# Optimization experiments

Hardware: AMD Instinct MI355X
Metric: run time of the kernel (lower is better)

## Reference

```python
import jax, jax.numpy as jnp
import numpy as np

H = 32          # query heads
KV = 8          # kv heads
DH = 64         # head dim
WINDOW = 1024   # sliding window
BASE = 10000.0  # rope base


def _rope(x, pos):
    """Interleaved RoPE as in RotaryEmbedding.apply. x: (B,H,T,Dh), pos: (T,)."""
    inv = 1.0 / (BASE ** (jnp.arange(0, DH, 2, dtype=jnp.float32) / DH))  # (Dh/2,)
    freqs = pos.astype(jnp.float32)[:, None] * inv[None, :]               # (T, Dh/2)
    cos = jnp.cos(freqs)[None, None].astype(x.dtype)
    sin = jnp.sin(freqs)[None, None].astype(x.dtype)
    x1, x2 = x[..., ::2], x[..., 1::2]
    o1 = x1 * cos - x2 * sin
    o2 = x1 * sin + x2 * cos
    return jnp.stack([o1, o2], axis=-1).reshape(x.shape)


def setup_inputs() -> dict:
    key = jax.random.key(0)
    ks = jax.random.split(key, 5)
    B, T, D, Tc = 2, 4096, 2048, 4096
    x = jax.random.normal(ks[0], (B, T, D), jnp.float32)
    k_cache = jax.random.normal(ks[1], (B, KV, Tc, DH), jnp.float32)
    v_cache = jax.random.normal(ks[2], (B, KV, Tc, DH), jnp.float32)
    Wq = jax.random.normal(ks[3], (D, D), jnp.float32) * 0.02
    Wo = jax.random.normal(ks[4], (D, D), jnp.float32) * 0.02
    return {"x": x, "k_cache": k_cache, "v_cache": v_cache, "Wq": Wq, "Wo": Wo}


def reference(x, k_cache, v_cache, Wq, Wo):
    """AttnLayer.forward, role='follower', local=True, return_attn=False, eval mode."""
    B, T, D = x.shape
    rep = H // KV
    # q projection: nn.Linear(d, H*Dh, bias=False) -> x @ W.T
    q = (x @ Wq.T).reshape(B, T, H, DH).transpose(0, 2, 1, 3)  # (B,H,T,Dh)
    Tc = k_cache.shape[2]
    pos_q = jnp.arange(Tc - T, Tc)
    q = _rope(q, pos_q)
    # GQA: KV -> H head replication (repeat_interleave along head dim)
    k = jnp.repeat(k_cache, rep, axis=1)  # (B,H,Tc,Dh)
    v = jnp.repeat(v_cache, rep, axis=1)
    # sliding-window slice: keep last `window` keys
    w = min(WINDOW, Tc)
    k = k[:, :, Tc - w:, :]  # (B,H,Tk,Dh)
    v = v[:, :, Tc - w:, :]
    Tk = w
    scale = 1.0 / np.sqrt(DH).astype(np.float32)
    scores = jnp.einsum('bhtd,bhsd->bhts', q, k) * scale  # (B,H,T,Tk)
    # torch SDPA is_causal with L != S uses a TOP-LEFT aligned tril mask: j <= i
    causal = jnp.arange(Tk)[None, :] <= jnp.arange(T)[:, None]  # (T,Tk)
    scores = jnp.where(causal[None, None], scores, -jnp.inf)
    attn = jax.nn.softmax(scores, axis=-1)
    out = jnp.einsum('bhts,bhsd->bhtd', attn, v)
    out = out.transpose(0, 2, 1, 3).reshape(B, T, H * DH)
    return out @ Wo.T
```

## Files before the change

kernel.cpp:

```cpp
#include <hip/hip_runtime.h>
#include <math.h>

typedef __attribute__((ext_vector_type(8))) short short8;
typedef __attribute__((ext_vector_type(4))) float floatx4;
typedef __attribute__((ext_vector_type(4))) unsigned int uintx4;
typedef __attribute__((ext_vector_type(2))) unsigned int uintx2;

#define MFMA16(a, b, c) __builtin_amdgcn_mfma_f32_16x16x32_bf16((a), (b), (c), 0, 0, 0)

#define QSCALE 0.18033688011112042f

__device__ __forceinline__ unsigned short f2bf(float x) {
    unsigned int u = __float_as_uint(x);
    u += 0x7fffu + ((u >> 16) & 1u);
    return (unsigned short)(u >> 16);
}

__device__ __forceinline__ short8 lds8(const unsigned short* p) {
    return *reinterpret_cast<const short8*>(p);
}

__device__ __forceinline__ void g2l16(const unsigned short* g, unsigned short* l) {
    __builtin_amdgcn_global_load_lds(
        (const __attribute__((address_space(1))) unsigned int*)g,
        (__attribute__((address_space(3))) unsigned int*)l,
        16, 0, 0);
}

__device__ __forceinline__ unsigned int cvtpk(float a, float b) {
    unsigned int r;
    asm("v_cvt_pk_bf16_f32 %0, %1, %2" : "=v"(r) : "v"(a), "v"(b));
    return r;
}

__device__ __forceinline__ void pl32swap(unsigned int& a, unsigned int& b) {
    asm("v_permlane32_swap_b32 %0, %1" : "+v"(a), "+v"(b));
}

__device__ __forceinline__ void pl16swap(unsigned int& a, unsigned int& b) {
    asm("v_permlane16_swap_b32 %0, %1" : "+v"(a), "+v"(b));
}

__global__ void cvt_bf16(const float* __restrict__ src, unsigned short* __restrict__ dst, int n4) {
    int i = blockIdx.x * blockDim.x + threadIdx.x;
    if (i >= n4) return;
    float4 v = reinterpret_cast<const float4*>(src)[i];
    ushort4 o;
    o.x = f2bf(v.x); o.y = f2bf(v.y); o.z = f2bf(v.z); o.w = f2bf(v.w);
    reinterpret_cast<ushort4*>(dst)[i] = o;
}

__global__ void prep_k(const float* __restrict__ kc, unsigned short* __restrict__ Kw) {
    int i = blockIdx.x * blockDim.x + threadIdx.x;
    int d4  = (i & 15) * 4;
    int s   = (i >> 4) & 1023;
    int bkv = i >> 14;
    size_t src = ((size_t)bkv * 4096 + 3072 + s) * 64 + d4;
    float4 kv = *reinterpret_cast<const float4*>(kc + src);
    ushort4 ko;
    ko.x = f2bf(kv.x); ko.y = f2bf(kv.y); ko.z = f2bf(kv.z); ko.w = f2bf(kv.w);
    *reinterpret_cast<ushort4*>(Kw + ((size_t)bkv * 1024 + s) * 64 + d4) = ko;
}

__global__ void prep_v(const float* __restrict__ vc, unsigned short* __restrict__ Vt) {
    __shared__ unsigned short tl[64][72];
    const int bkv = blockIdx.x >> 4;
    const int s0  = (blockIdx.x & 15) * 64;
    const int t   = threadIdx.x;
    const int sl  = t >> 2;
    const int dq  = (t & 3) * 16;
    const float* src = vc + ((size_t)bkv * 4096 + 3072 + s0 + sl) * 64 + dq;
    float4 v0 = reinterpret_cast<const float4*>(src)[0];
    float4 v1 = reinterpret_cast<const float4*>(src)[1];
    float4 v2 = reinterpret_cast<const float4*>(src)[2];
    float4 v3 = reinterpret_cast<const float4*>(src)[3];
    tl[dq +  0][sl] = f2bf(v0.x); tl[dq +  1][sl] = f2bf(v0.y);
    tl[dq +  2][sl] = f2bf(v0.z); tl[dq +  3][sl] = f2bf(v0.w);
    tl[dq +  4][sl] = f2bf(v1.x); tl[dq +  5][sl] = f2bf(v1.y);
    tl[dq +  6][sl] = f2bf(v1.z); tl[dq +  7][sl] = f2bf(v1.w);
    tl[dq +  8][sl] = f2bf(v2.x); tl[dq +  9][sl] = f2bf(v2.y);
    tl[dq + 10][sl] = f2bf(v2.z); tl[dq + 11][sl] = f2bf(v2.w);
    tl[dq + 12][sl] = f2bf(v3.x); tl[dq + 13][sl] = f2bf(v3.y);
    tl[dq + 14][sl] = f2bf(v3.z); tl[dq + 15][sl] = f2bf(v3.w);
    __syncthreads();
    const int dl = t >> 2;
    const int sc = (t & 3) * 16;
    unsigned short* dst = Vt + ((size_t)bkv * 64 + dl) * 1024 + s0 + sc;
    short8 x0 = *reinterpret_cast<const short8*>(&tl[dl][sc]);
    short8 x1 = *reinterpret_cast<const short8*>(&tl[dl][sc + 8]);
    *reinterpret_cast<short8*>(dst)     = x0;
    *reinterpret_cast<short8*>(dst + 8) = x1;
}

template <int EPI>
__global__ __launch_bounds__(512, 2)
void gemm256(const unsigned short* __restrict__ A,
             const unsigned short* __restrict__ Bt,
             float* __restrict__ Cf,
             unsigned short* __restrict__ Cb) {
    constexpr int K  = 2048;
    constexpr int NT = 64;
    __shared__ unsigned short sm[32768];

    const int tid  = threadIdx.x;
    const int lane = tid & 63;
    const int l15  = lane & 15;
    const int quad = lane >> 4;
    const int wid  = tid >> 6;
    const int wr   = wid >> 2;
    const int wc   = wid & 3;

    const int bn = blockIdx.x & 7;
    const int bm = blockIdx.x >> 3;

    const unsigned short* gA0 = A  + (size_t)(bm * 256 + 2 * wid * 16 + l15) * K + quad * 8;
    const unsigned short* gA1 = gA0 + (size_t)16 * K;
    const unsigned short* gB0 = Bt + (size_t)(bn * 256 + 2 * wid * 16 + l15) * K + quad * 8;
    const unsigned short* gB1 = gB0 + (size_t)16 * K;

    auto STAGE = [&](int t) {
        unsigned short* dst = sm + (t & 1) * 16384 + 2 * wid * 512;
        const int off = t * 32;
        g2l16(gA0 + off, dst);
        g2l16(gA1 + off, dst + 512);
        g2l16(gB0 + off, dst + 8192);
        g2l16(gB1 + off, dst + 8704);
    };

    floatx4 acc[8][4];
#pragma unroll
    for (int i = 0; i < 8; ++i)
#pragma unroll
        for (int j = 0; j < 4; ++j) acc[i][j] = floatx4{0, 0, 0, 0};

    STAGE(0);
    STAGE(1);
    asm volatile("s_waitcnt vmcnt(4)" ::: "memory");
    __builtin_amdgcn_s_barrier();
    asm volatile("" ::: "memory");

    for (int t = 0; t < NT; ++t) {
        const unsigned short* cb = sm + (t & 1) * 16384;

        short8 bf[4], af[8];
#pragma unroll
        for (int j = 0; j < 4; ++j)
            bf[j] = lds8(cb + 8192 + (wc * 4 + j) * 512 + lane * 8);
#pragma unroll
        for (int i = 0; i < 8; ++i)
            af[i] = lds8(cb + (wr * 8 + i) * 512 + lane * 8);

        asm volatile("s_waitcnt lgkmcnt(0)" ::: "memory");
        __builtin_amdgcn_s_barrier();
        asm volatile("" ::: "memory");

        if (t + 2 < NT) STAGE(t + 2);

        __builtin_amdgcn_s_setprio(1);
#pragma unroll
        for (int i = 0; i < 8; ++i)
#pragma unroll
            for (int j = 0; j < 4; ++j)
                acc[i][j] = MFMA16(af[i], bf[j], acc[i][j]);
        __builtin_amdgcn_s_setprio(0);

        if (t + 2 < NT) asm volatile("s_waitcnt vmcnt(4)" ::: "memory");
        else            asm volatile("s_waitcnt vmcnt(0)" ::: "memory");
        __builtin_amdgcn_s_barrier();
        asm volatile("" ::: "memory");
    }

    float2* tabf = reinterpret_cast<float2*>(sm);
    if (EPI == 0) {
        const int t0 = (bm & 15) * 256;
        for (int e = tid; e < 8192; e += 512) {
            int tl = e >> 5, d2 = e & 31;
            float f = (float)(t0 + tl) * exp2f(-(float)d2 * 0.41524101186092f);
            float sn, cs; __sincosf(f, &sn, &cs);
            tabf[tl * 32 + d2] = make_float2(cs, sn);
        }
        __syncthreads();
    }

#pragma unroll
    for (int i = 0; i < 8; ++i)
#pragma unroll
        for (int j = 0; j < 4; ++j)
#pragma unroll
            for (int r = 0; r < 4; ++r) {
                int row = bm * 256 + wr * 128 + i * 16 + quad * 4 + r;
                int col = bn * 256 + wc * 64 + j * 16 + l15;
                float v = acc[i][j][r];
                if (EPI == 0) {
                    float p = __shfl_xor(v, 1);
                    int t_ = row & 4095, b_ = row >> 12;
                    int hh = col >> 6, d = col & 63;
                    int tl = wr * 128 + i * 16 + quad * 4 + r;
                    float2 cspair = tabf[tl * 32 + (d >> 1)];
                    float o = (d & 1) ? (p * cspair.y + v * cspair.x)
                                      : (v * cspair.x - p * cspair.y);
                    o *= QSCALE;
                    float po = __shfl_xor(o, 1);
                    if (!(lane & 1)) {
                        unsigned int pk = (unsigned int)f2bf(o) |
                                          ((unsigned int)f2bf(po) << 16);
                        *reinterpret_cast<unsigned int*>(
                            Cb + ((size_t)((b_ * 32 + hh) * 4096 + t_)) * 64 + d) = pk;
                    }
                } else {
                    Cf[(size_t)row * 2048 + col] = v;
                }
            }
}

__global__ __launch_bounds__(512, 8)
void attn(const unsigned short* __restrict__ Q,
          const unsigned short* __restrict__ Kw,
          const unsigned short* __restrict__ Vt,
          unsigned short* __restrict__ O) {
    const int blk  = blockIdx.x;
    const int qblk = blk & 31;
    const int bh   = blk >> 5;
    const int h    = bh & 31;
    const int b    = bh >> 5;
    const int kvh  = h >> 2;

    const int tid  = threadIdx.x;
    const int lane = tid & 63;
    const int l15  = lane & 15;
    const int quad = lane >> 4;
    const int wid  = tid >> 6;
    const int qt0  = qblk * 128 + wid * 16;

    const unsigned short* Qp = Q  + ((size_t)bh * 4096 + qt0) * 64;
    const unsigned short* Kp = Kw + (size_t)(b * 8 + kvh) * 1024 * 64;
    const unsigned short* Vp = Vt + (size_t)(b * 8 + kvh) * 64 * 1024;

    __shared__ unsigned short Ks[2][4096];
    __shared__ unsigned short Vs[2][4096];

    short8 qa0 = lds8(&Qp[l15 * 64 + quad * 8]);
    short8 qa1 = lds8(&Qp[l15 * 64 + 32 + quad * 8]);

    short8 ones;
#pragma unroll
    for (int i = 0; i < 8; ++i) ones[i] = (short)0x3F80;

    const unsigned short* gK = Kp + (size_t)((wid >> 1) * 16 + l15) * 64
                                  + (wid & 1) * 32 + quad * 8;
    const unsigned short* gV = Vp + (size_t)((wid >> 1) * 16 + l15) * 1024
                                  + (wid & 1) * 32 + quad * 8;
    unsigned short* sK0 = &Ks[0][wid * 512];
    unsigned short* sK1 = &Ks[1][wid * 512];
    unsigned short* sV0 = &Vs[0][wid * 512];
    unsigned short* sV1 = &Vs[1][wid * 512];

    const int ntiles = (qblk < 7 ? 2 * qblk + 2 : 16);
    const int nkW    = (qt0 + 16 < 1024) ? qt0 + 16 : 1024;
    const int ntW    = (nkW + 63) >> 6;
    const bool diagW = (qt0 < 1024);

    g2l16(gK, sK0);
    g2l16(gV, sV0);

    floatx4 o0 = {0,0,0,0}, o1 = {0,0,0,0}, o2 = {0,0,0,0}, o3 = {0,0,0,0};
    floatx4 La = {0,0,0,0};
    float m = -INFINITY;

    for (int it = 0; it < ntiles; ++it) {
        __syncthreads();
        const int cur = it & 1;
        if (it + 1 < ntiles) {
            g2l16(gK + (it + 1) * 4096, cur ? sK0 : sK1);
            g2l16(gV + (it + 1) * 64,   cur ? sV0 : sV1);
        }
        if (it >= ntW) continue;
        const int s0 = it << 6;
        const unsigned short* Kc = Ks[cur];
        const unsigned short* Vc = Vs[cur];

        floatx4 sS[4];
        __builtin_amdgcn_s_setprio(1);
#pragma unroll
        for (int c = 0; c < 4; ++c) {
            floatx4 z = {0, 0, 0, 0};
            z = MFMA16(lds8(Kc + c * 1024 + lane * 8), qa0, z);
            z = MFMA16(lds8(Kc + c * 1024 + 512 + lane * 8), qa1, z);
            sS[c] = z;
        }
        __builtin_amdgcn_s_setprio(0);

        const bool last = (it == ntW - 1);
        bool skipHi = false;
        if (last && diagW) {
#pragma unroll
            for (int c = 0; c < 4; ++c)
#pragma unroll
                for (int r = 0; r < 4; ++r)
                    if (s0 + c * 16 + quad * 4 + r > qt0 + l15) sS[c][r] = -INFINITY;
            skipHi = (nkW - s0 <= 32);
        }

        float t0 = fmaxf(fmaxf(sS[0][0], sS[0][1]), fmaxf(sS[0][2], sS[0][3]));
        float t1 = fmaxf(fmaxf(sS[1][0], sS[1][1]), fmaxf(sS[1][2], sS[1][3]));
        float t2 = fmaxf(fmaxf(sS[2][0], sS[2][1]), fmaxf(sS[2][2], sS[2][3]));
        float t3 = fmaxf(fmaxf(sS[3][0], sS[3][1]), fmaxf(sS[3][2], sS[3][3]));
        float mx = fmaxf(fmaxf(t0, t1), fmaxf(t2, t3));
        mx = fmaxf(mx, __shfl_xor(mx, 16));
        mx = fmaxf(mx, __shfl_xor(mx, 32));

        if (!__all(mx <= m + 8.0f)) {
            const float mn = fmaxf(m, mx);
            const float alpha = exp2f(m - mn);
            m = mn;
            o0 *= alpha; o1 *= alpha; o2 *= alpha; o3 *= alpha;
            La *= alpha;
        }

        float p[4][4];
#pragma unroll
        for (int c = 0; c < 4; ++c)
#pragma unroll
            for (int r = 0; r < 4; ++r) p[c][r] = exp2f(sS[c][r] - m);

        unsigned int a0 = cvtpk(p[0][0], p[0][1]);
        unsigned int a1 = cvtpk(p[0][2], p[0][3]);
        unsigned int a2 = cvtpk(p[1][0], p[1][1]);
        unsigned int a3 = cvtpk(p[1][2], p[1][3]);
        pl32swap(a0, a2); pl32swap(a1, a3);
        pl16swap(a0, a2); pl16swap(a1, a3);
        uintx4 tlo = {a0, a1, a2, a3};
        short8 pa_lo = __builtin_bit_cast(short8, tlo);

        __builtin_amdgcn_s_setprio(1);
        o0 = MFMA16(lds8(Vc + 0 * 512 + lane * 8), pa_lo, o0);
        o1 = MFMA16(lds8(Vc + 2 * 512 + lane * 8), pa_lo, o1);
        o2 = MFMA16(lds8(Vc + 4 * 512 + lane * 8), pa_lo, o2);
        o3 = MFMA16(lds8(Vc + 6 * 512 + lane * 8), pa_lo, o3);
        La = MFMA16(ones, pa_lo, La);
        __builtin_amdgcn_s_setprio(0);
        if (!skipHi) {
            unsigned int b0 = cvtpk(p[2][0], p[2][1]);
            unsigned int b1 = cvtpk(p[2][2], p[2][3]);
            unsigned int b2 = cvtpk(p[3][0], p[3][1]);
            unsigned int b3 = cvtpk(p[3][2], p[3][3]);
            pl32swap(b0, b2); pl32swap(b1, b3);
            pl16swap(b0, b2); pl16swap(b1, b3);
            uintx4 thi = {b0, b1, b2, b3};
            short8 pa_hi = __builtin_bit_cast(short8, thi);
            __builtin_amdgcn_s_setprio(1);
            o0 = MFMA16(lds8(Vc + 1 * 512 + lane * 8), pa_hi, o0);
            o1 = MFMA16(lds8(Vc + 3 * 512 + lane * 8), pa_hi, o1);
            o2 = MFMA16(lds8(Vc + 5 * 512 + lane * 8), pa_hi, o2);
            o3 = MFMA16(lds8(Vc + 7 * 512 + lane * 8), pa_hi, o3);
            La = MFMA16(ones, pa_hi, La);
            __builtin_amdgcn_s_setprio(0);
        }
    }

    const float inv = 1.f / La[0];

    unsigned short* Op = O + (size_t)b * 4096 * 2048 + (size_t)(qt0 + l15) * 2048
                           + h * 64 + quad * 4;
    uintx2 w0, w1, w2, w3;
    w0.x = cvtpk(o0[0] * inv, o0[1] * inv); w0.y = cvtpk(o0[2] * inv, o0[3] * inv);
    w1.x = cvtpk(o1[0] * inv, o1[1] * inv); w1.y = cvtpk(o1[2] * inv, o1[3] * inv);
    w2.x = cvtpk(o2[0] * inv, o2[1] * inv); w2.y = cvtpk(o2[2] * inv, o2[3] * inv);
    w3.x = cvtpk(o3[0] * inv, o3[1] * inv); w3.y = cvtpk(o3[2] * inv, o3[3] * inv);
    *reinterpret_cast<uintx2*>(Op)      = w0;
    *reinterpret_cast<uintx2*>(Op + 16) = w1;
    *reinterpret_cast<uintx2*>(Op + 32) = w2;
    *reinterpret_cast<uintx2*>(Op + 48) = w3;
}

extern "C" void kernel_launch(void* const* d_in, const int* in_sizes, int n_in,
                              void* d_out, int out_size, void* d_ws, size_t ws_size,
                              hipStream_t stream) {
    const float* x  = (const float*)d_in[0];
    const float* kc = (const float*)d_in[1];
    const float* vc = (const float*)d_in[2];
    const float* Wq = (const float*)d_in[3];
    const float* Wo = (const float*)d_in[4];
    float* out = (float*)d_out;

    char* ws = (char*)d_ws;
    unsigned short* Xb  = (unsigned short*)(ws);
    unsigned short* Qb  = (unsigned short*)(ws + 33554432);
    unsigned short* Wqb = (unsigned short*)(ws + 67108864);
    unsigned short* Wob = (unsigned short*)(ws + 75497472);
    unsigned short* Kwb = (unsigned short*)(ws + 83886080);
    unsigned short* Vtb = (unsigned short*)(ws + 85983232);

    cvt_bf16<<<16384, 256, 0, stream>>>(x,  Xb,  4194304);
    cvt_bf16<<<4096,  256, 0, stream>>>(Wq, Wqb, 1048576);
    cvt_bf16<<<4096,  256, 0, stream>>>(Wo, Wob, 1048576);
    prep_k<<<1024, 256, 0, stream>>>(kc, Kwb);
    prep_v<<<256, 256, 0, stream>>>(vc, Vtb);

    gemm256<0><<<256, 512, 0, stream>>>(Xb, Wqb, nullptr, Qb);
    attn<<<2048, 512, 0, stream>>>(Qb, Kwb, Vtb, Xb);
    gemm256<1><<<256, 512, 0, stream>>>(Xb, Wob, out, nullptr);
}
```

Measured before the change: 442.2 us.

## Restructure GEMM main loop into finer-grained interleaved load/MFMA stages with 64-wide K tiles

```diff
diff --git a/kernel.cpp b/kernel.cpp
--- a/kernel.cpp
+++ b/kernel.cpp
@@ -94,13 +94,13 @@
 
 template <int EPI>
 __global__ __launch_bounds__(512, 2)
-void gemm256(const unsigned short* __restrict__ A,
-             const unsigned short* __restrict__ Bt,
-             float* __restrict__ Cf,
-             unsigned short* __restrict__ Cb) {
-    constexpr int K  = 2048;
-    constexpr int NT = 64;
-    __shared__ unsigned short sm[32768];
+void gemmk(const unsigned short* __restrict__ A,
+           const unsigned short* __restrict__ Bt,
+           float* __restrict__ Cf,
+           unsigned short* __restrict__ Cb) {
+    constexpr int K   = 2048;
+    constexpr int NKT = 32;
+    __shared__ __align__(16) unsigned short sm[65536];
 
     const int tid  = threadIdx.x;
     const int lane = tid & 63;
@@ -113,19 +113,13 @@
     const int bn = blockIdx.x & 7;
     const int bm = blockIdx.x >> 3;
 
-    const unsigned short* gA0 = A  + (size_t)(bm * 256 + 2 * wid * 16 + l15) * K + quad * 8;
-    const unsigned short* gA1 = gA0 + (size_t)16 * K;
-    const unsigned short* gB0 = Bt + (size_t)(bn * 256 + 2 * wid * 16 + l15) * K + quad * 8;
-    const unsigned short* gB1 = gB0 + (size_t)16 * K;
-
-    auto STAGE = [&](int t) {
-        unsigned short* dst = sm + (t & 1) * 16384 + 2 * wid * 512;
-        const int off = t * 32;
-        g2l16(gA0 + off, dst);
-        g2l16(gA1 + off, dst + 512);
-        g2l16(gB0 + off, dst + 8192);
-        g2l16(gB1 + off, dst + 8704);
-    };
+    const unsigned short* gAl = A  + (size_t)(bm * 256 + l15) * K + quad * 8;
+    const unsigned short* gBl = Bt + (size_t)(bn * 256 + l15) * K + quad * 8;
+
+#define STG_A(kt, kh, c) g2l16(gAl + (size_t)((c) * 8 + wid) * 16 * K + (kt) * 64 + (kh) * 32, \
+                               sm + ((kt) & 1) * 16384 + (kh) * 8192 + ((c) * 8 + wid) * 512)
+#define STG_B(kt, kh, c) g2l16(gBl + (size_t)((c) * 8 + wid) * 16 * K + (kt) * 64 + (kh) * 32, \
+                               sm + 32768 + ((kt) & 1) * 16384 + (kh) * 8192 + ((c) * 8 + wid) * 512)
 
     floatx4 acc[8][4];
 #pragma unroll
@@ -133,42 +127,110 @@
 #pragma unroll
         for (int j = 0; j < 4; ++j) acc[i][j] = floatx4{0, 0, 0, 0};
 
-    STAGE(0);
-    STAGE(1);
-    asm volatile("s_waitcnt vmcnt(4)" ::: "memory");
+    STG_B(0, 0, 0); STG_B(0, 0, 1); STG_A(0, 0, 0); STG_A(0, 0, 1);
+    STG_B(0, 1, 0); STG_B(0, 1, 1); STG_A(0, 1, 0); STG_A(0, 1, 1);
+    STG_B(1, 0, 0); STG_B(1, 0, 1); STG_A(1, 0, 0); STG_A(1, 0, 1);
+    asm volatile("s_waitcnt vmcnt(8)" ::: "memory");
     __builtin_amdgcn_s_barrier();
     asm volatile("" ::: "memory");
 
-    for (int t = 0; t < NT; ++t) {
-        const unsigned short* cb = sm + (t & 1) * 16384;
-
-        short8 bf[4], af[8];
-#pragma unroll
-        for (int j = 0; j < 4; ++j)
-            bf[j] = lds8(cb + 8192 + (wc * 4 + j) * 512 + lane * 8);
-#pragma unroll
-        for (int i = 0; i < 8; ++i)
-            af[i] = lds8(cb + (wr * 8 + i) * 512 + lane * 8);
-
-        asm volatile("s_waitcnt lgkmcnt(0)" ::: "memory");
-        __builtin_amdgcn_s_barrier();
-        asm volatile("" ::: "memory");
-
-        if (t + 2 < NT) STAGE(t + 2);
-
-        __builtin_amdgcn_s_setprio(1);
-#pragma unroll
-        for (int i = 0; i < 8; ++i)
-#pragma unroll
-            for (int j = 0; j < 4; ++j)
-                acc[i][j] = MFMA16(af[i], bf[j], acc[i][j]);
-        __builtin_amdgcn_s_setprio(0);
-
-        if (t + 2 < NT) asm volatile("s_waitcnt vmcnt(4)" ::: "memory");
-        else            asm volatile("s_waitcnt vmcnt(0)" ::: "memory");
-        __builtin_amdgcn_s_barrier();
-        asm volatile("" ::: "memory");
+#define DO_MFMA(ip)                                                  \
+    __builtin_amdgcn_s_setprio(1);                                   \
+    acc[2*(ip)][0]   = MFMA16(af0, bf[0], acc[2*(ip)][0]);           \
+    acc[2*(ip)][1]   = MFMA16(af0, bf[1], acc[2*(ip)][1]);           \
+    acc[2*(ip)][2]   = MFMA16(af0, bf[2], acc[2*(ip)][2]);           \
+    acc[2*(ip)][3]   = MFMA16(af0, bf[3], acc[2*(ip)][3]);           \
+    acc[2*(ip)+1][0] = MFMA16(af1, bf[0], acc[2*(ip)+1][0]);         \
+    acc[2*(ip)+1][1] = MFMA16(af1, bf[1], acc[2*(ip)+1][1]);         \
+    acc[2*(ip)+1][2] = MFMA16(af1, bf[2], acc[2*(ip)+1][2]);         \
+    acc[2*(ip)+1][3] = MFMA16(af1, bf[3], acc[2*(ip)+1][3]);         \
+    __builtin_amdgcn_s_setprio(0);
+
+#define BAR()   { __builtin_amdgcn_s_barrier(); asm volatile("" ::: "memory"); }
+#define LGKM0() asm volatile("s_waitcnt lgkmcnt(0)" ::: "memory")
+
+    for (int kt = 0; kt < NKT; ++kt) {
+        const int d = kt & 1;
+        const unsigned short* Ab = sm + d * 16384;
+        const unsigned short* Bb = sm + 32768 + d * 16384;
+        const bool s1 = (kt + 1 < NKT);
+        const bool s2 = (kt + 2 < NKT);
+        short8 af0, af1, bf[4];
+
+        bf[0] = lds8(Bb + (wc * 4 + 0) * 512 + lane * 8);
+        bf[1] = lds8(Bb + (wc * 4 + 1) * 512 + lane * 8);
+        bf[2] = lds8(Bb + (wc * 4 + 2) * 512 + lane * 8);
+        bf[3] = lds8(Bb + (wc * 4 + 3) * 512 + lane * 8);
+        af0   = lds8(Ab + (wr * 8 + 0) * 512 + lane * 8);
+        af1   = lds8(Ab + (wr * 8 + 1) * 512 + lane * 8);
+        if (s1) STG_B(kt + 1, 1, 0);
+        BAR(); LGKM0();
+        DO_MFMA(0);
+        BAR();
+
+        af0 = lds8(Ab + (wr * 8 + 2) * 512 + lane * 8);
+        af1 = lds8(Ab + (wr * 8 + 3) * 512 + lane * 8);
+        if (s1) STG_B(kt + 1, 1, 1);
+        BAR(); LGKM0();
+        DO_MFMA(1);
+        BAR();
+
+        af0 = lds8(Ab + (wr * 8 + 4) * 512 + lane * 8);
+        af1 = lds8(Ab + (wr * 8 + 5) * 512 + lane * 8);
+        if (s1) STG_A(kt + 1, 1, 0);
+        BAR(); LGKM0();
+        DO_MFMA(2);
+        BAR();
+
+        af0 = lds8(Ab + (wr * 8 + 6) * 512 + lane * 8);
+        af1 = lds8(Ab + (wr * 8 + 7) * 512 + lane * 8);
+        if (s1) STG_A(kt + 1, 1, 1);
+        BAR(); LGKM0();
+        DO_MFMA(3);
+        if (s1) asm volatile("s_waitcnt vmcnt(8)" ::: "memory");
+        else    asm volatile("s_waitcnt vmcnt(0)" ::: "memory");
+        BAR();
+
+        bf[0] = lds8(Bb + 8192 + (wc * 4 + 0) * 512 + lane * 8);
+        bf[1] = lds8(Bb + 8192 + (wc * 4 + 1) * 512 + lane * 8);
+        bf[2] = lds8(Bb + 8192 + (wc * 4 + 2) * 512 + lane * 8);
+        bf[3] = lds8(Bb + 8192 + (wc * 4 + 3) * 512 + lane * 8);
+        af0   = lds8(Ab + 8192 + (wr * 8 + 0) * 512 + lane * 8);
+        af1   = lds8(Ab + 8192 + (wr * 8 + 1) * 512 + lane * 8);
+        if (s2) STG_B(kt + 2, 0, 0);
+        BAR(); LGKM0();
+        DO_MFMA(0);
+        BAR();
+
+        af0 = lds8(Ab + 8192 + (wr * 8 + 2) * 512 + lane * 8);
+        af1 = lds8(Ab + 8192 + (wr * 8 + 3) * 512 + lane * 8);
+        if (s2) STG_B(kt + 2, 0, 1);
+        BAR(); LGKM0();
+        DO_MFMA(1);
+        BAR();
+
+        af0 = lds8(Ab + 8192 + (wr * 8 + 4) * 512 + lane * 8);
+        af1 = lds8(Ab + 8192 + (wr * 8 + 5) * 512 + lane * 8);
+        if (s2) STG_A(kt + 2, 0, 0);
+        BAR(); LGKM0();
+        DO_MFMA(2);
+        BAR();
+
+        af0 = lds8(Ab + 8192 + (wr * 8 + 6) * 512 + lane * 8);
+        af1 = lds8(Ab + 8192 + (wr * 8 + 7) * 512 + lane * 8);
+        if (s2) STG_A(kt + 2, 0, 1);
+        BAR(); LGKM0();
+        DO_MFMA(3);
+        if (s2)      asm volatile("s_waitcnt vmcnt(8)" ::: "memory");
+        else if (s1) asm volatile("s_waitcnt vmcnt(4)" ::: "memory");
+        else         asm volatile("s_waitcnt vmcnt(0)" ::: "memory");
+        BAR();
     }
+#undef STG_A
+#undef STG_B
+#undef DO_MFMA
+#undef BAR
+#undef LGKM0
 
     float2* tabf = reinterpret_cast<float2*>(sm);
     if (EPI == 0) {
@@ -397,7 +459,7 @@
     prep_k<<<1024, 256, 0, stream>>>(kc, Kwb);
     prep_v<<<256, 256, 0, stream>>>(vc, Vtb);
 
-    gemm256<0><<<256, 512, 0, stream>>>(Xb, Wqb, nullptr, Qb);
+    gemmk<0><<<256, 512, 0, stream>>>(Xb, Wqb, nullptr, Qb);
     attn<<<2048, 512, 0, stream>>>(Qb, Kwb, Vtb, Xb);
-    gemm256<1><<<256, 512, 0, stream>>>(Xb, Wob, out, nullptr);
-}
+    gemmk<1><<<256, 512, 0, stream>>>(Xb, Wob, out, nullptr);
+}
```

After: 442.0 us. Within noise of the previous version (-0.0%).

## Shrink GEMM tile to 128x256 for more blocks and split attention launch

Applied to the files above, without the earlier changes.

```diff
diff --git a/kernel.cpp b/kernel.cpp
--- a/kernel.cpp
+++ b/kernel.cpp
@@ -93,14 +93,14 @@
 }
 
 template <int EPI>
-__global__ __launch_bounds__(512, 2)
-void gemm256(const unsigned short* __restrict__ A,
+__global__ __launch_bounds__(512, 4)
+void gemm128(const unsigned short* __restrict__ A,
              const unsigned short* __restrict__ Bt,
              float* __restrict__ Cf,
              unsigned short* __restrict__ Cb) {
     constexpr int K  = 2048;
     constexpr int NT = 64;
-    __shared__ unsigned short sm[32768];
+    __shared__ __align__(16) unsigned short sm[24576];
 
     const int tid  = threadIdx.x;
     const int lane = tid & 63;
@@ -113,42 +113,40 @@
     const int bn = blockIdx.x & 7;
     const int bm = blockIdx.x >> 3;
 
-    const unsigned short* gA0 = A  + (size_t)(bm * 256 + 2 * wid * 16 + l15) * K + quad * 8;
-    const unsigned short* gA1 = gA0 + (size_t)16 * K;
-    const unsigned short* gB0 = Bt + (size_t)(bn * 256 + 2 * wid * 16 + l15) * K + quad * 8;
-    const unsigned short* gB1 = gB0 + (size_t)16 * K;
+    const unsigned short* gA0 = A  + (size_t)(bm * 128 + wid * 16 + l15) * K + quad * 8;
+    const unsigned short* gB0 = Bt + (size_t)(bn * 256 + wid * 16 + l15) * K + quad * 8;
+    const unsigned short* gB1 = gB0 + (size_t)128 * K;
 
     auto STAGE = [&](int t) {
-        unsigned short* dst = sm + (t & 1) * 16384 + 2 * wid * 512;
+        unsigned short* dst = sm + (t & 1) * 12288;
         const int off = t * 32;
-        g2l16(gA0 + off, dst);
-        g2l16(gA1 + off, dst + 512);
-        g2l16(gB0 + off, dst + 8192);
-        g2l16(gB1 + off, dst + 8704);
+        g2l16(gA0 + off, dst + wid * 512);
+        g2l16(gB0 + off, dst + 4096 + wid * 512);
+        g2l16(gB1 + off, dst + 8192 + wid * 512);
     };
 
-    floatx4 acc[8][4];
-#pragma unroll
-    for (int i = 0; i < 8; ++i)
+    floatx4 acc[4][4];
+#pragma unroll
+    for (int i = 0; i < 4; ++i)
 #pragma unroll
         for (int j = 0; j < 4; ++j) acc[i][j] = floatx4{0, 0, 0, 0};
 
     STAGE(0);
     STAGE(1);
-    asm volatile("s_waitcnt vmcnt(4)" ::: "memory");
+    asm volatile("s_waitcnt vmcnt(3)" ::: "memory");
     __builtin_amdgcn_s_barrier();
     asm volatile("" ::: "memory");
 
     for (int t = 0; t < NT; ++t) {
-        const unsigned short* cb = sm + (t & 1) * 16384;
-
-        short8 bf[4], af[8];
+        const unsigned short* cb = sm + (t & 1) * 12288;
+
+        short8 af[4], bf[4];
+#pragma unroll
+        for (int i = 0; i < 4; ++i)
+            af[i] = lds8(cb + (wr * 4 + i) * 512 + lane * 8);
 #pragma unroll
         for (int j = 0; j < 4; ++j)
-            bf[j] = lds8(cb + 8192 + (wc * 4 + j) * 512 + lane * 8);
-#pragma unroll
-        for (int i = 0; i < 8; ++i)
-            af[i] = lds8(cb + (wr * 8 + i) * 512 + lane * 8);
+            bf[j] = lds8(cb + 4096 + (wc * 4 + j) * 512 + lane * 8);
 
         asm volatile("s_waitcnt lgkmcnt(0)" ::: "memory");
         __builtin_amdgcn_s_barrier();
@@ -158,13 +156,13 @@
 
         __builtin_amdgcn_s_setprio(1);
 #pragma unroll
-        for (int i = 0; i < 8; ++i)
+        for (int i = 0; i < 4; ++i)
 #pragma unroll
             for (int j = 0; j < 4; ++j)
                 acc[i][j] = MFMA16(af[i], bf[j], acc[i][j]);
         __builtin_amdgcn_s_setprio(0);
 
-        if (t + 2 < NT) asm volatile("s_waitcnt vmcnt(4)" ::: "memory");
+        if (t + 2 < NT) asm volatile("s_waitcnt vmcnt(3)" ::: "memory");
         else            asm volatile("s_waitcnt vmcnt(0)" ::: "memory");
         __builtin_amdgcn_s_barrier();
         asm volatile("" ::: "memory");
@@ -172,8 +170,8 @@
 
     float2* tabf = reinterpret_cast<float2*>(sm);
     if (EPI == 0) {
-        const int t0 = (bm & 15) * 256;
-        for (int e = tid; e < 8192; e += 512) {
+        const int t0 = (bm & 31) * 128;
+        for (int e = tid; e < 4096; e += 512) {
             int tl = e >> 5, d2 = e & 31;
             float f = (float)(t0 + tl) * exp2f(-(float)d2 * 0.41524101186092f);
             float sn, cs; __sincosf(f, &sn, &cs);
@@ -183,19 +181,19 @@
     }
 
 #pragma unroll
-    for (int i = 0; i < 8; ++i)
+    for (int i = 0; i < 4; ++i)
 #pragma unroll
         for (int j = 0; j < 4; ++j)
 #pragma unroll
             for (int r = 0; r < 4; ++r) {
-                int row = bm * 256 + wr * 128 + i * 16 + quad * 4 + r;
+                int row = bm * 128 + wr * 64 + i * 16 + quad * 4 + r;
                 int col = bn * 256 + wc * 64 + j * 16 + l15;
                 float v = acc[i][j][r];
                 if (EPI == 0) {
                     float p = __shfl_xor(v, 1);
                     int t_ = row & 4095, b_ = row >> 12;
                     int hh = col >> 6, d = col & 63;
-                    int tl = wr * 128 + i * 16 + quad * 4 + r;
+                    int tl = wr * 64 + i * 16 + quad * 4 + r;
                     float2 cspair = tabf[tl * 32 + (d >> 1)];
                     float o = (d & 1) ? (p * cspair.y + v * cspair.x)
                                       : (v * cspair.x - p * cspair.y);
@@ -217,8 +215,8 @@
 void attn(const unsigned short* __restrict__ Q,
           const unsigned short* __restrict__ Kw,
           const unsigned short* __restrict__ Vt,
-          unsigned short* __restrict__ O) {
-    const int blk  = blockIdx.x;
+          unsigned short* __restrict__ O, int base) {
+    const int blk  = blockIdx.x + base;
     const int qblk = blk & 31;
     const int bh   = blk >> 5;
     const int h    = bh & 31;
@@ -397,7 +395,8 @@
     prep_k<<<1024, 256, 0, stream>>>(kc, Kwb);
     prep_v<<<256, 256, 0, stream>>>(vc, Vtb);
 
-    gemm256<0><<<256, 512, 0, stream>>>(Xb, Wqb, nullptr, Qb);
-    attn<<<2048, 512, 0, stream>>>(Qb, Kwb, Vtb, Xb);
-    gemm256<1><<<256, 512, 0, stream>>>(Xb, Wob, out, nullptr);
-}
+    gemm128<0><<<512, 512, 0, stream>>>(Xb, Wqb, nullptr, Qb);
+    attn<<<1024, 512, 0, stream>>>(Qb, Kwb, Vtb, Xb, 0);
+    attn<<<1024, 512, 0, stream>>>(Qb, Kwb, Vtb, Xb, 1024);
+    gemm128<1><<<512, 512, 0, stream>>>(Xb, Wob, out, nullptr);
+}
```

New measurement: 497.0 us. 12.4% more time.
